# Optimization experiments

Hardware: AMD Instinct MI355X
Metric: run time of the kernel (lower is better)

Reference implementation:

```python
import jax, jax.numpy as jnp
import numpy as np

HEADS = 20          # 1280 / 64 head_dim, standard SD UNet attention
LORA_SCALE = 1.0    # lora_scale init arg


def setup_inputs() -> dict:
    key = jax.random.key(0)
    ks = jax.random.split(key, 16)
    def w(k, shape, s=0.02):
        return jax.random.normal(k, shape, dtype=jnp.float32) * s
    H, C, R = 1280, 768, 64  # hidden_size, cross_attention_dim, lora_rank
    return {
        "hidden_states": jax.random.normal(ks[0], (16, 4096, H), dtype=jnp.float32),
        "encoder_hidden_states": jax.random.normal(ks[1], (16, 77, C), dtype=jnp.float32),
        # base attention projections (diffusers: q/k/v no bias, to_out has bias)
        "Wq": w(ks[2], (H, H)), "Wk": w(ks[3], (C, H)), "Wv": w(ks[4], (C, H)),
        "Wo": w(ks[5], (H, H)), "bo": jnp.zeros((H,), dtype=jnp.float32),
        # LoRA adapters (down: in->rank, up: rank->out, no bias)
        "q_down": w(ks[6], (H, R)), "q_up": w(ks[7], (R, H)),
        "k_down": w(ks[8], (C, R)), "k_up": w(ks[9], (R, H)),
        "v_down": w(ks[10], (C, R)), "v_up": w(ks[11], (R, H)),
        "o_down": w(ks[12], (H, R)), "o_up": w(ks[13], (R, H)),
    }


def reference(hidden_states, encoder_hidden_states, Wq, Wk, Wv, Wo, bo,
              q_down, q_up, k_down, k_up, v_down, v_up, o_down, o_up):
    b, sq, _ = hidden_states.shape
    # base projections + LoRA low-rank corrections
    q = hidden_states @ Wq + LORA_SCALE * ((hidden_states @ q_down) @ q_up)
    k = encoder_hidden_states @ Wk + LORA_SCALE * ((encoder_hidden_states @ k_down) @ k_up)
    v = encoder_hidden_states @ Wv + LORA_SCALE * ((encoder_hidden_states @ v_down) @ v_up)

    d = q.shape[-1] // HEADS
    def split_heads(x):  # [b, s, h*d] -> [b, h, s, d]
        return x.reshape(x.shape[0], x.shape[1], HEADS, d).transpose(0, 2, 1, 3)
    qh, kh, vh = split_heads(q), split_heads(k), split_heads(v)

    # scaled dot-product attention (no mask, non-causal, dropout=0)
    scale = 1.0 / np.sqrt(d).astype(np.float32)
    scores = jnp.einsum('bhqd,bhkd->bhqk', qh, kh) * scale
    probs = jax.nn.softmax(scores, axis=-1)
    attn_out = jnp.einsum('bhqk,bhkd->bhqd', probs, vh)
    attn_out = attn_out.transpose(0, 2, 1, 3).reshape(b, sq, HEADS * d)

    # output projection + LoRA on W_O
    out = attn_out @ Wo + bo + LORA_SCALE * ((attn_out @ o_down) @ o_up)
    return out
```

## Files before the change

kernel.cpp:

```cpp
#include <hip/hip_runtime.h>
#include <stdint.h>

typedef unsigned short u16;
typedef __attribute__((ext_vector_type(8))) short short8;
typedef __attribute__((ext_vector_type(4))) float f32x4;

__device__ __forceinline__ u16 f2bf(float f) {
  union { float f; unsigned u; } v; v.f = f;
  unsigned r = v.u + 0x7fffu + ((v.u >> 16) & 1u);
  return (u16)(r >> 16);
}

__device__ __forceinline__ void g2lds16(const u16* g, u16* l) {
  __builtin_amdgcn_global_load_lds(
      (const __attribute__((address_space(1))) uint32_t*)g,
      (__attribute__((address_space(3))) uint32_t*)l, 16, 0, 0);
}

#define BAR()   asm volatile("s_barrier" ::: "memory")
#define LGKM0() asm volatile("s_waitcnt lgkmcnt(0)" ::: "memory")
#define VM8()   asm volatile("s_waitcnt vmcnt(8)" ::: "memory")
#define VM0()   asm volatile("s_waitcnt vmcnt(0)" ::: "memory")
#define PRIO1() __builtin_amdgcn_s_setprio(1)
#define PRIO0() __builtin_amdgcn_s_setprio(0)

__global__ __launch_bounds__(256) void k_convert(const float* __restrict__ in,
                                                 u16* __restrict__ out, int n8) {
  int i = blockIdx.x * 256 + threadIdx.x;
  if (i >= n8) return;
  const float4* p = (const float4*)(in + (size_t)i * 8);
  float4 a = p[0], b = p[1];
  short8 o;
  o[0] = (short)f2bf(a.x); o[1] = (short)f2bf(a.y);
  o[2] = (short)f2bf(a.z); o[3] = (short)f2bf(a.w);
  o[4] = (short)f2bf(b.x); o[5] = (short)f2bf(b.y);
  o[6] = (short)f2bf(b.z); o[7] = (short)f2bf(b.w);
  *(short8*)(out + (size_t)i * 8) = o;
}

__global__ __launch_bounds__(256) void k_convert_pad(const float* __restrict__ in,
                                                     u16* __restrict__ out,
                                                     int n8_valid, int n8_total) {
  int i = blockIdx.x * 256 + threadIdx.x;
  if (i >= n8_total) return;
  short8 o;
  if (i < n8_valid) {
    const float4* p = (const float4*)(in + (size_t)i * 8);
    float4 a = p[0], b = p[1];
    o[0] = (short)f2bf(a.x); o[1] = (short)f2bf(a.y);
    o[2] = (short)f2bf(a.z); o[3] = (short)f2bf(a.w);
    o[4] = (short)f2bf(b.x); o[5] = (short)f2bf(b.y);
    o[6] = (short)f2bf(b.z); o[7] = (short)f2bf(b.w);
  } else {
#pragma unroll
    for (int e = 0; e < 8; ++e) o[e] = 0;
  }
  *(short8*)(out + (size_t)i * 8) = o;
}

__global__ __launch_bounds__(256) void k_fusew(const float* __restrict__ W,
                                               const float* __restrict__ dn_g,
                                               const float* __restrict__ up_g,
                                               u16* __restrict__ Wt, int K, int N) {
  __shared__ float dn[64][65];
  __shared__ float up[64][17];
  const int k0 = blockIdx.x * 64, n0 = blockIdx.y * 16;
  const int kc = threadIdx.x & 63, ty = threadIdx.x >> 6;
  for (int c = threadIdx.x; c < 4096; c += 256)
    dn[c >> 6][c & 63] = dn_g[(size_t)(k0 + (c >> 6)) * 64 + (c & 63)];
  for (int c = threadIdx.x; c < 1024; c += 256)
    up[c >> 4][c & 15] = up_g[(size_t)(c >> 4) * N + n0 + (c & 15)];
  __syncthreads();
  float acc[4];
#pragma unroll
  for (int e = 0; e < 4; ++e)
    acc[e] = W[(size_t)(k0 + kc) * N + n0 + ty * 4 + e];
#pragma unroll 16
  for (int r = 0; r < 64; ++r) {
    float d = dn[kc][r];
#pragma unroll
    for (int e = 0; e < 4; ++e) acc[e] += d * up[r][ty * 4 + e];
  }
#pragma unroll
  for (int e = 0; e < 4; ++e)
    Wt[(size_t)(n0 + ty * 4 + e) * K + k0 + kc] = f2bf(acc[e]);
}

template <int OUT_MODE>
__global__ __launch_bounds__(256) void k_gemm(const u16* __restrict__ A,
                                              const u16* __restrict__ Bt,
                                              void* __restrict__ Cout,
                                              const float* __restrict__ bias,
                                              int M, int N, int K) {
  __shared__ __align__(16) u16 As[128 * 32];
  __shared__ __align__(16) u16 Bs[128 * 32];
  const int tid = threadIdx.x, lane = tid & 63, w = tid >> 6;
  const int n0 = blockIdx.x * 128, m0 = blockIdx.y * 128;
  const int wm = (w >> 1) * 64, wn = (w & 1) * 64;

  f32x4 acc[4][4];
  f32x4 zf = {0.f, 0.f, 0.f, 0.f};
#pragma unroll
  for (int i = 0; i < 4; ++i)
#pragma unroll
    for (int j = 0; j < 4; ++j) acc[i][j] = zf;

  const int c0 = w, c1 = w + 4;
  const int rA0 = c0 * 16 + (lane >> 2), rA1 = c1 * 16 + (lane >> 2);
  const int kp = (lane & 3) * 8;
  const u16* gA0 = A + (size_t)(m0 + rA0) * K + kp;
  const u16* gA1 = A + (size_t)(m0 + rA1) * K + kp;
  const u16* gB0 = Bt + (size_t)(n0 + rA0) * K + kp;
  const u16* gB1 = Bt + (size_t)(n0 + rA1) * K + kp;
  u16* lA0 = As + c0 * 512;  u16* lA1 = As + c1 * 512;
  u16* lB0 = Bs + c0 * 512;  u16* lB1 = Bs + c1 * 512;

  const int fr = lane & 15, kg = (lane >> 4) * 8;

  for (int k0 = 0; k0 < K; k0 += 32) {
    g2lds16(gA0 + k0, lA0);
    g2lds16(gA1 + k0, lA1);
    g2lds16(gB0 + k0, lB0);
    g2lds16(gB1 + k0, lB1);
    __syncthreads();
    short8 af[4], bf[4];
#pragma unroll
    for (int i = 0; i < 4; ++i)
      af[i] = *(const short8*)(As + (wm + i * 16 + fr) * 32 + kg);
#pragma unroll
    for (int j = 0; j < 4; ++j)
      bf[j] = *(const short8*)(Bs + (wn + j * 16 + fr) * 32 + kg);
#pragma unroll
    for (int i = 0; i < 4; ++i)
#pragma unroll
      for (int j = 0; j < 4; ++j)
        acc[i][j] = __builtin_amdgcn_mfma_f32_16x16x32_bf16(af[i], bf[j], acc[i][j], 0, 0, 0);
    __syncthreads();
  }

  const int rb = (lane >> 4) * 4;
  if (OUT_MODE == 0) {
    u16* C = (u16*)Cout;
#pragma unroll
    for (int i = 0; i < 4; ++i)
#pragma unroll
      for (int j = 0; j < 4; ++j) {
        int col = n0 + wn + j * 16 + fr;
#pragma unroll
        for (int r = 0; r < 4; ++r) {
          int row = m0 + wm + i * 16 + rb + r;
          C[(size_t)row * N + col] = f2bf(acc[i][j][r]);
        }
      }
  } else {
    float* C = (float*)Cout;
#pragma unroll
    for (int i = 0; i < 4; ++i)
#pragma unroll
      for (int j = 0; j < 4; ++j) {
        int col = n0 + wn + j * 16 + fr;
        float bj = bias[col];
#pragma unroll
        for (int r = 0; r < 4; ++r) {
          int row = m0 + wm + i * 16 + rb + r;
          C[(size_t)row * N + col] = acc[i][j][r] + bj;
        }
      }
  }
}


#define GEMM256_SETUP(A_, Bt_)                                                 \
  constexpr int K = 1280;                                                      \
  constexpr int N = 1280;                                                      \
  __shared__ __align__(16) u16 lds[2][2][2][128 * 64];                         \
  const int tid = threadIdx.x, lane = tid & 63, w = tid >> 6;                  \
  const int bid = blockIdx.x;                                                  \
  const int tile = (bid & 7) * 160 + (bid >> 3);                               \
  const int n0 = (tile % 5) * 256, m0 = (tile / 5) * 256;                      \
  const int l0 = w * 2;                                                        \
  const u16* gsrc[8];                                                          \
  _Pragma("unroll") for (int s = 0; s < 8; ++s) {                              \
    const int side = s >> 2, h = (s >> 1) & 1, l = s & 1;                      \
    const int o = (l0 + l) * 1024 + lane * 16;                                 \
    const int row = o >> 7;                                                    \
    const int scol = (o & 127) ^ ((row & 7) << 4);                             \
    const u16* base = side ? ((Bt_) + (size_t)(n0 + h * 128 + row) * K)        \
                           : ((A_) + (size_t)(m0 + h * 128 + row) * K);        \
    gsrc[s] = base + (scol >> 1);                                              \
  }                                                                            \
  const int fr = lane & 15;                                                    \
  const int q16b = (lane >> 4) * 16;                                           \
  const int xr = (fr & 7) << 4;                                                \
  const int cT0 = ((0 + q16b) ^ xr) >> 1;                                      \
  const int cT1 = ((64 + q16b) ^ xr) >> 1;                                     \
  const int ha = w >> 2;                                                       \
  const int hb = (w & 3) >> 1;                                                 \
  const int rB0 = (w & 1) * 64;

#define STAGE(P, KT)                                                           \
  do {                                                                         \
    _Pragma("unroll") for (int s = 0; s < 8; ++s) {                            \
      const int side = s >> 2, h = (s >> 1) & 1, l = s & 1;                    \
      g2lds16(gsrc[s] + (KT) * 64, &lds[P][side][h][(l0 + l) * 512]);          \
    }                                                                          \
  } while (0)

#define LOAD_AF(P, IB)                                                         \
  do {                                                                         \
    _Pragma("unroll") for (int ii = 0; ii < 4; ++ii) {                         \
      const u16* rp = &lds[P][0][ha][(((IB) + ii) * 16 + fr) * 64];            \
      af[ii][0] = *(const short8*)(rp + cT0);                                  \
      af[ii][1] = *(const short8*)(rp + cT1);                                  \
    }                                                                          \
  } while (0)

#define LOAD_BF(P, JB)                                                         \
  do {                                                                         \
    _Pragma("unroll") for (int jj = 0; jj < 2; ++jj) {                         \
      const u16* rp = &lds[P][1][hb][(rB0 + ((JB) + jj) * 16 + fr) * 64];      \
      bf[(JB) + jj][0] = *(const short8*)(rp + cT0);                           \
      bf[(JB) + jj][1] = *(const short8*)(rp + cT1);                           \
    }                                                                          \
  } while (0)

#define MFMA_Q(IO, JB)                                                         \
  do {                                                                         \
    _Pragma("unroll") for (int t = 0; t < 2; ++t)                              \
        _Pragma("unroll") for (int ii = 0; ii < 4; ++ii)                       \
            _Pragma("unroll") for (int jj = 0; jj < 2; ++jj)                   \
                acc[(IO) + ii][(JB) + jj] =                                    \
        __builtin_amdgcn_mfma_f32_16x16x32_bf16(                               \
            af[ii][t], bf[(JB) + jj][t], acc[(IO) + ii][(JB) + jj], 0, 0, 0);  \
  } while (0)

#define GEMM256_EPI()                                                          \
  const int rb = (lane >> 4) * 4;                                              \
  const int orow = m0 + (w >> 2) * 128;                                        \
  const int ocol = n0 + (w & 3) * 64;                                          \
  if (OUT_MODE == 0) {                                                         \
    u16* C = (u16*)Cout;                                                       \
    _Pragma("unroll") for (int i = 0; i < 8; ++i)                              \
        _Pragma("unroll") for (int j = 0; j < 4; ++j) {                        \
      const int col = ocol + j * 16 + fr;                                      \
      _Pragma("unroll") for (int r = 0; r < 4; ++r) {                          \
        const int row = orow + i * 16 + rb + r;                                \
        C[(size_t)row * N + col] = f2bf(acc[i][j][r]);                         \
      }                                                                        \
    }                                                                          \
  } else {                                                                     \
    float* C = (float*)Cout;                                                   \
    _Pragma("unroll") for (int i = 0; i < 8; ++i)                              \
        _Pragma("unroll") for (int j = 0; j < 4; ++j) {                        \
      const int col = ocol + j * 16 + fr;                                      \
      const float bj = bias[col];                                              \
      _Pragma("unroll") for (int r = 0; r < 4; ++r) {                          \
        const int row = orow + i * 16 + rb + r;                                \
        C[(size_t)row * N + col] = acc[i][j][r] + bj;                          \
      }                                                                        \
    }                                                                          \
  }

template <int OUT_MODE>
__global__ __launch_bounds__(512, 2) void k_gemm256(const u16* __restrict__ A,
                                                    const u16* __restrict__ Bt,
                                                    void* __restrict__ Cout,
                                                    const float* __restrict__ bias) {
  GEMM256_SETUP(A, Bt);

  short8 af[4][2], bf[4][2];
  f32x4 acc[8][4];
  {
    f32x4 zf = {0.f, 0.f, 0.f, 0.f};
#pragma unroll
    for (int i = 0; i < 8; ++i)
#pragma unroll
      for (int j = 0; j < 4; ++j) acc[i][j] = zf;
  }

  STAGE(0, 0);
  STAGE(1, 1);
  VM8();
  BAR();

  for (int it = 0; it < 10; ++it) {
    const bool last = (it == 9);
    LOAD_AF(0, 0); LOAD_BF(0, 0);
    BAR(); LGKM0(); PRIO1(); MFMA_Q(0, 0); PRIO0(); BAR();
    LOAD_BF(0, 2);
    BAR(); LGKM0(); PRIO1(); MFMA_Q(0, 2); PRIO0(); BAR();
    LOAD_AF(0, 4);
    BAR(); LGKM0(); PRIO1(); MFMA_Q(4, 2); PRIO0(); BAR();
    if (!last) STAGE(0, 2 * it + 2);
    BAR(); PRIO1(); MFMA_Q(4, 0); PRIO0();
    if (!last) { VM8(); } else { VM0(); }
    BAR();
    LOAD_AF(1, 0); LOAD_BF(1, 0);
    BAR(); LGKM0(); PRIO1(); MFMA_Q(0, 0); PRIO0(); BAR();
    LOAD_BF(1, 2);
    BAR(); LGKM0(); PRIO1(); MFMA_Q(0, 2); PRIO0(); BAR();
    LOAD_AF(1, 4);
    BAR(); LGKM0(); PRIO1(); MFMA_Q(4, 2); PRIO0(); BAR();
    if (!last) STAGE(1, 2 * it + 3);
    BAR(); PRIO1(); MFMA_Q(4, 0); PRIO0();
    if (!last) { VM8(); }
    BAR();
  }

  GEMM256_EPI();
}

template <int OUT_MODE>
__global__ __launch_bounds__(512, 2) void k_gemm256f(const u16* __restrict__ A,
                                                     const u16* __restrict__ Bt,
                                                     void* __restrict__ Cout,
                                                     const float* __restrict__ bias) {
  GEMM256_SETUP(A, Bt);

  short8 af[4][2], bf[4][2];
  f32x4 acc[8][4];
  {
    f32x4 zf = {0.f, 0.f, 0.f, 0.f};
#pragma unroll
    for (int i = 0; i < 8; ++i)
#pragma unroll
      for (int j = 0; j < 4; ++j) acc[i][j] = zf;
  }

  STAGE(0, 0);
  STAGE(1, 1);
  VM8();
  BAR();

  for (int t = 0; t < 20; ++t) {
    const int P = t & 1;
    LOAD_AF(P, 0);
    LOAD_BF(P, 0);
    LOAD_BF(P, 2);
    MFMA_Q(0, 0);
    MFMA_Q(0, 2);
    LOAD_AF(P, 4);
    MFMA_Q(4, 2);
    LGKM0();
    BAR();
    if (t < 18) STAGE(P, t + 2);
    PRIO1(); MFMA_Q(4, 0); PRIO0();
    if (t < 18) { VM8(); } else { VM0(); }
    BAR();
  }

  GEMM256_EPI();
}

__global__ __launch_bounds__(256) void k_attn(u16* __restrict__ Q,
                                              const u16* __restrict__ Kb,
                                              const u16* __restrict__ Vb) {
  const int mt = blockIdx.x, h = blockIdx.y, b = blockIdx.z;
  const int tid = threadIdx.x, lane = tid & 63, w = tid >> 6;
  const int m0 = b * 4096 + mt * 128;
  const int ccol = h * 64;

  __shared__ __align__(16) u16 Kl[80 * 72];
  __shared__ __align__(16) u16 Vt[64 * 104];
  __shared__ __align__(16) u16 Pl[128 * 104];

  {
    short8 z;
#pragma unroll
    for (int e = 0; e < 8; ++e) z[e] = 0;
    for (int i = tid; i < 720; i += 256)  ((short8*)Kl)[i] = z;
    for (int i = tid; i < 832; i += 256)  ((short8*)Vt)[i] = z;
    for (int i = tid; i < 1664; i += 256) ((short8*)Pl)[i] = z;
  }
  __syncthreads();

  for (int c = tid; c < 616; c += 256) {
    int s = c >> 3, d0 = (c & 7) * 8;
    short8 v = *(const short8*)(Kb + (size_t)(b * 77 + s) * 1280 + ccol + d0);
    *(short8*)(Kl + s * 72 + d0) = v;
  }
  for (int c = tid; c < 616; c += 256) {
    int s = c >> 3, d0 = (c & 7) * 8;
    short8 v = *(const short8*)(Vb + (size_t)(b * 77 + s) * 1280 + ccol + d0);
#pragma unroll
    for (int e = 0; e < 8; ++e) Vt[(d0 + e) * 104 + s] = (u16)v[e];
  }

  const int cb = lane & 15, kg = (lane >> 4) * 8;
  short8 qf[2][2];
#pragma unroll
  for (int i = 0; i < 2; ++i)
#pragma unroll
    for (int t = 0; t < 2; ++t) {
      int row = m0 + w * 32 + i * 16 + cb;
      qf[i][t] = *(const short8*)(Q + (size_t)row * 1280 + ccol + t * 32 + kg);
    }
  __syncthreads();

  f32x4 sc[2][5];
  {
    f32x4 zf = {0.f, 0.f, 0.f, 0.f};
#pragma unroll
    for (int i = 0; i < 2; ++i)
#pragma unroll
      for (int j = 0; j < 5; ++j) sc[i][j] = zf;
  }
#pragma unroll
  for (int t = 0; t < 2; ++t) {
    short8 kf[5];
#pragma unroll
    for (int j = 0; j < 5; ++j)
      kf[j] = *(const short8*)(Kl + (j * 16 + cb) * 72 + t * 32 + kg);
#pragma unroll
    for (int i = 0; i < 2; ++i)
#pragma unroll
      for (int j = 0; j < 5; ++j)
        sc[i][j] = __builtin_amdgcn_mfma_f32_16x16x32_bf16(qf[i][t], kf[j], sc[i][j], 0, 0, 0);
  }

  float inv[2][4];
#pragma unroll
  for (int i = 0; i < 2; ++i) {
#pragma unroll
    for (int r = 0; r < 4; ++r) {
      float m = -1e30f;
#pragma unroll
      for (int j = 0; j < 5; ++j) {
        float s = sc[i][j][r] * 0.125f;
        sc[i][j][r] = s;
        if (j * 16 + cb < 77) m = fmaxf(m, s);
      }
#pragma unroll
      for (int mk = 8; mk >= 1; mk >>= 1) m = fmaxf(m, __shfl_xor(m, mk, 64));
      float sum = 0.f;
#pragma unroll
      for (int j = 0; j < 5; ++j) {
        float pv = (j * 16 + cb < 77) ? __expf(sc[i][j][r] - m) : 0.f;
        sc[i][j][r] = pv;
        sum += pv;
      }
#pragma unroll
      for (int mk = 8; mk >= 1; mk >>= 1) sum += __shfl_xor(sum, mk, 64);
      inv[i][r] = 1.f / sum;
    }
  }

  {
    int rbase = (lane >> 4) * 4;
#pragma unroll
    for (int i = 0; i < 2; ++i)
#pragma unroll
      for (int j = 0; j < 5; ++j)
#pragma unroll
        for (int r = 0; r < 4; ++r)
          Pl[(w * 32 + i * 16 + rbase + r) * 104 + j * 16 + cb] = f2bf(sc[i][j][r]);
  }
  __syncthreads();

  f32x4 o[2][4];
  {
    f32x4 zf = {0.f, 0.f, 0.f, 0.f};
#pragma unroll
    for (int i = 0; i < 2; ++i)
#pragma unroll
      for (int n = 0; n < 4; ++n) o[i][n] = zf;
  }
#pragma unroll
  for (int t = 0; t < 3; ++t) {
    short8 pf[2], vf[4];
#pragma unroll
    for (int i = 0; i < 2; ++i)
      pf[i] = *(const short8*)(Pl + (w * 32 + i * 16 + cb) * 104 + t * 32 + kg);
#pragma unroll
    for (int n = 0; n < 4; ++n)
      vf[n] = *(const short8*)(Vt + (n * 16 + cb) * 104 + t * 32 + kg);
#pragma unroll
    for (int i = 0; i < 2; ++i)
#pragma unroll
      for (int n = 0; n < 4; ++n)
        o[i][n] = __builtin_amdgcn_mfma_f32_16x16x32_bf16(pf[i], vf[n], o[i][n], 0, 0, 0);
  }

  {
    int rbase = (lane >> 4) * 4;
#pragma unroll
    for (int i = 0; i < 2; ++i)
#pragma unroll
      for (int n = 0; n < 4; ++n)
#pragma unroll
        for (int r = 0; r < 4; ++r) {
          int row = m0 + w * 32 + i * 16 + rbase + r;
          Q[(size_t)row * 1280 + ccol + n * 16 + cb] = f2bf(o[i][n][r] * inv[i][r]);
        }
  }
}

extern "C" void kernel_launch(void* const* d_in, const int* in_sizes, int n_in,
                              void* d_out, int out_size, void* d_ws, size_t ws_size,
                              hipStream_t stream) {
  (void)in_sizes; (void)n_in; (void)out_size; (void)ws_size;
  const float* hs  = (const float*)d_in[0];
  const float* ehs = (const float*)d_in[1];
  const float* Wq  = (const float*)d_in[2];
  const float* Wk  = (const float*)d_in[3];
  const float* Wv  = (const float*)d_in[4];
  const float* Wo  = (const float*)d_in[5];
  const float* bo  = (const float*)d_in[6];
  const float* qd  = (const float*)d_in[7];
  const float* qu  = (const float*)d_in[8];
  const float* kd  = (const float*)d_in[9];
  const float* ku  = (const float*)d_in[10];
  const float* vd  = (const float*)d_in[11];
  const float* vu  = (const float*)d_in[12];
  const float* od  = (const float*)d_in[13];
  const float* ou  = (const float*)d_in[14];

  char* p = (char*)d_ws;
  u16* q_buf = (u16*)p;  p += (size_t)65536 * 1280 * 2;
  u16* wq_t  = (u16*)p;  p += (size_t)1280 * 1280 * 2;
  u16* wo_t  = (u16*)p;  p += (size_t)1280 * 1280 * 2;
  u16* wk_t  = (u16*)p;  p += (size_t)1280 * 768 * 2;
  u16* wv_t  = (u16*)p;  p += (size_t)1280 * 768 * 2;
  u16* ehs_b = (u16*)p;  p += (size_t)1280 * 768 * 2;
  u16* k_buf = (u16*)p;  p += (size_t)1280 * 1280 * 2;
  u16* v_buf = (u16*)p;  p += (size_t)1280 * 1280 * 2;
  u16* hs_b  = (u16*)d_out;

  k_convert<<<40960, 256, 0, stream>>>(hs, hs_b, 10485760);
  k_convert_pad<<<480, 256, 0, stream>>>(ehs, ehs_b, 118272, 122880);

  k_fusew<<<dim3(20, 80), 256, 0, stream>>>(Wq, qd, qu, wq_t, 1280, 1280);
  k_fusew<<<dim3(12, 80), 256, 0, stream>>>(Wk, kd, ku, wk_t, 768, 1280);
  k_fusew<<<dim3(12, 80), 256, 0, stream>>>(Wv, vd, vu, wv_t, 768, 1280);
  k_fusew<<<dim3(20, 80), 256, 0, stream>>>(Wo, od, ou, wo_t, 1280, 1280);

  k_gemm256f<0><<<1280, 512, 0, stream>>>(hs_b, wq_t, q_buf, nullptr);
  k_gemm<0><<<dim3(10, 10), 256, 0, stream>>>(ehs_b, wk_t, k_buf, nullptr, 1280, 1280, 768);
  k_gemm<0><<<dim3(10, 10), 256, 0, stream>>>(ehs_b, wv_t, v_buf, nullptr, 1280, 1280, 768);

  k_attn<<<dim3(32, 20, 16), 256, 0, stream>>>(q_buf, k_buf, v_buf);

  k_gemm256<1><<<1280, 512, 0, stream>>>(q_buf, wo_t, d_out, bo);
}
```

Baseline: 803.2 us.

## Fuse fp32-to-bf16 conversion into Q GEMM and fold softmax scale into Q

Removes the standalone hidden_states conversion kernel by having the Q projection GEMM load fp32 A tiles, convert them to bf16 in registers, and write them to LDS. The softmax scale and log2(e) factor are applied in the Q GEMM epilogue, so the attention kernel can use exp2f without the row-max reduction. This cuts a full pass over the large input. Risks are a slower A-load path than direct global-to-LDS loads, and possible overflow because the max subtraction is gone.

```diff
diff --git a/kernel.cpp b/kernel.cpp
--- a/kernel.cpp
+++ b/kernel.cpp
@@ -1,4 +1,5 @@
 #include <hip/hip_runtime.h>
+#include <hip/hip_bf16.h>
 #include <stdint.h>
 
 typedef unsigned short u16;
@@ -9,6 +10,13 @@
   union { float f; unsigned u; } v; v.f = f;
   unsigned r = v.u + 0x7fffu + ((v.u >> 16) & 1u);
   return (u16)(r >> 16);
+}
+
+__device__ __forceinline__ unsigned pkbf2(float lo, float hi) {
+  __hip_bfloat162 h2 = __float22bfloat162_rn(make_float2(lo, hi));
+  unsigned u;
+  __builtin_memcpy(&u, &h2, sizeof(u));
+  return u;
 }
 
 __device__ __forceinline__ void g2lds16(const u16* g, u16* l) {
@@ -24,19 +32,7 @@
 #define PRIO1() __builtin_amdgcn_s_setprio(1)
 #define PRIO0() __builtin_amdgcn_s_setprio(0)
 
-__global__ __launch_bounds__(256) void k_convert(const float* __restrict__ in,
-                                                 u16* __restrict__ out, int n8) {
-  int i = blockIdx.x * 256 + threadIdx.x;
-  if (i >= n8) return;
-  const float4* p = (const float4*)(in + (size_t)i * 8);
-  float4 a = p[0], b = p[1];
-  short8 o;
-  o[0] = (short)f2bf(a.x); o[1] = (short)f2bf(a.y);
-  o[2] = (short)f2bf(a.z); o[3] = (short)f2bf(a.w);
-  o[4] = (short)f2bf(b.x); o[5] = (short)f2bf(b.y);
-  o[6] = (short)f2bf(b.z); o[7] = (short)f2bf(b.w);
-  *(short8*)(out + (size_t)i * 8) = o;
-}
+#define QSCALE 0.18033688f
 
 __global__ __launch_bounds__(256) void k_convert_pad(const float* __restrict__ in,
                                                      u16* __restrict__ out,
@@ -170,25 +166,15 @@
 }
 
 
-#define GEMM256_SETUP(A_, Bt_)                                                 \
+#define GEMM256_TILE_RD()                                                      \
   constexpr int K = 1280;                                                      \
   constexpr int N = 1280;                                                      \
   __shared__ __align__(16) u16 lds[2][2][2][128 * 64];                         \
-  const int tid = threadIdx.x, lane = tid & 63, w = tid >> 6;                  \
+  const int lane = threadIdx.x & 63, w = threadIdx.x >> 6;                     \
   const int bid = blockIdx.x;                                                  \
   const int tile = (bid & 7) * 160 + (bid >> 3);                               \
   const int n0 = (tile % 5) * 256, m0 = (tile / 5) * 256;                      \
   const int l0 = w * 2;                                                        \
-  const u16* gsrc[8];                                                          \
-  _Pragma("unroll") for (int s = 0; s < 8; ++s) {                              \
-    const int side = s >> 2, h = (s >> 1) & 1, l = s & 1;                      \
-    const int o = (l0 + l) * 1024 + lane * 16;                                 \
-    const int row = o >> 7;                                                    \
-    const int scol = (o & 127) ^ ((row & 7) << 4);                             \
-    const u16* base = side ? ((Bt_) + (size_t)(n0 + h * 128 + row) * K)        \
-                           : ((A_) + (size_t)(m0 + h * 128 + row) * K);        \
-    gsrc[s] = base + (scol >> 1);                                              \
-  }                                                                            \
   const int fr = lane & 15;                                                    \
   const int q16b = (lane >> 4) * 16;                                           \
   const int xr = (fr & 7) << 4;                                                \
@@ -198,14 +184,6 @@
   const int hb = (w & 3) >> 1;                                                 \
   const int rB0 = (w & 1) * 64;
 
-#define STAGE(P, KT)                                                           \
-  do {                                                                         \
-    _Pragma("unroll") for (int s = 0; s < 8; ++s) {                            \
-      const int side = s >> 2, h = (s >> 1) & 1, l = s & 1;                    \
-      g2lds16(gsrc[s] + (KT) * 64, &lds[P][side][h][(l0 + l) * 512]);          \
-    }                                                                          \
-  } while (0)
-
 #define LOAD_AF(P, IB)                                                         \
   do {                                                                         \
     _Pragma("unroll") for (int ii = 0; ii < 4; ++ii) {                         \
@@ -234,98 +212,42 @@
             af[ii][t], bf[(JB) + jj][t], acc[(IO) + ii][(JB) + jj], 0, 0, 0);  \
   } while (0)
 
-#define GEMM256_EPI()                                                          \
-  const int rb = (lane >> 4) * 4;                                              \
-  const int orow = m0 + (w >> 2) * 128;                                        \
-  const int ocol = n0 + (w & 3) * 64;                                          \
-  if (OUT_MODE == 0) {                                                         \
-    u16* C = (u16*)Cout;                                                       \
+#define ACC_ZERO()                                                             \
+  do {                                                                         \
+    f32x4 zf = {0.f, 0.f, 0.f, 0.f};                                           \
     _Pragma("unroll") for (int i = 0; i < 8; ++i)                              \
-        _Pragma("unroll") for (int j = 0; j < 4; ++j) {                        \
-      const int col = ocol + j * 16 + fr;                                      \
-      _Pragma("unroll") for (int r = 0; r < 4; ++r) {                          \
-        const int row = orow + i * 16 + rb + r;                                \
-        C[(size_t)row * N + col] = f2bf(acc[i][j][r]);                         \
-      }                                                                        \
-    }                                                                          \
-  } else {                                                                     \
-    float* C = (float*)Cout;                                                   \
-    _Pragma("unroll") for (int i = 0; i < 8; ++i)                              \
-        _Pragma("unroll") for (int j = 0; j < 4; ++j) {                        \
-      const int col = ocol + j * 16 + fr;                                      \
-      const float bj = bias[col];                                              \
-      _Pragma("unroll") for (int r = 0; r < 4; ++r) {                          \
-        const int row = orow + i * 16 + rb + r;                                \
-        C[(size_t)row * N + col] = acc[i][j][r] + bj;                          \
-      }                                                                        \
-    }                                                                          \
-  }
-
-template <int OUT_MODE>
-__global__ __launch_bounds__(512, 2) void k_gemm256(const u16* __restrict__ A,
-                                                    const u16* __restrict__ Bt,
-                                                    void* __restrict__ Cout,
-                                                    const float* __restrict__ bias) {
-  GEMM256_SETUP(A, Bt);
-
-  short8 af[4][2], bf[4][2];
-  f32x4 acc[8][4];
-  {
-    f32x4 zf = {0.f, 0.f, 0.f, 0.f};
-#pragma unroll
-    for (int i = 0; i < 8; ++i)
-#pragma unroll
-      for (int j = 0; j < 4; ++j) acc[i][j] = zf;
-  }
-
-  STAGE(0, 0);
-  STAGE(1, 1);
-  VM8();
-  BAR();
-
-  for (int it = 0; it < 10; ++it) {
-    const bool last = (it == 9);
-    LOAD_AF(0, 0); LOAD_BF(0, 0);
-    BAR(); LGKM0(); PRIO1(); MFMA_Q(0, 0); PRIO0(); BAR();
-    LOAD_BF(0, 2);
-    BAR(); LGKM0(); PRIO1(); MFMA_Q(0, 2); PRIO0(); BAR();
-    LOAD_AF(0, 4);
-    BAR(); LGKM0(); PRIO1(); MFMA_Q(4, 2); PRIO0(); BAR();
-    if (!last) STAGE(0, 2 * it + 2);
-    BAR(); PRIO1(); MFMA_Q(4, 0); PRIO0();
-    if (!last) { VM8(); } else { VM0(); }
-    BAR();
-    LOAD_AF(1, 0); LOAD_BF(1, 0);
-    BAR(); LGKM0(); PRIO1(); MFMA_Q(0, 0); PRIO0(); BAR();
-    LOAD_BF(1, 2);
-    BAR(); LGKM0(); PRIO1(); MFMA_Q(0, 2); PRIO0(); BAR();
-    LOAD_AF(1, 4);
-    BAR(); LGKM0(); PRIO1(); MFMA_Q(4, 2); PRIO0(); BAR();
-    if (!last) STAGE(1, 2 * it + 3);
-    BAR(); PRIO1(); MFMA_Q(4, 0); PRIO0();
-    if (!last) { VM8(); }
-    BAR();
-  }
-
-  GEMM256_EPI();
-}
+        _Pragma("unroll") for (int j = 0; j < 4; ++j) acc[i][j] = zf;          \
+  } while (0)
 
 template <int OUT_MODE>
 __global__ __launch_bounds__(512, 2) void k_gemm256f(const u16* __restrict__ A,
                                                      const u16* __restrict__ Bt,
                                                      void* __restrict__ Cout,
                                                      const float* __restrict__ bias) {
-  GEMM256_SETUP(A, Bt);
+  GEMM256_TILE_RD();
+  const u16* gsrc[8];
+#pragma unroll
+  for (int s = 0; s < 8; ++s) {
+    const int side = s >> 2, h = (s >> 1) & 1, l = s & 1;
+    const int o = (l0 + l) * 1024 + lane * 16;
+    const int row = o >> 7;
+    const int scol = (o & 127) ^ ((row & 7) << 4);
+    const u16* base = side ? (Bt + (size_t)(n0 + h * 128 + row) * K)
+                           : (A + (size_t)(m0 + h * 128 + row) * K);
+    gsrc[s] = base + (scol >> 1);
+  }
+
+#define STAGE(P, KT)                                                           \
+  do {                                                                         \
+    _Pragma("unroll") for (int s = 0; s < 8; ++s) {                            \
+      const int side = s >> 2, h = (s >> 1) & 1, l = s & 1;                    \
+      g2lds16(gsrc[s] + (KT) * 64, &lds[P][side][h][(l0 + l) * 512]);          \
+    }                                                                          \
+  } while (0)
 
   short8 af[4][2], bf[4][2];
   f32x4 acc[8][4];
-  {
-    f32x4 zf = {0.f, 0.f, 0.f, 0.f};
-#pragma unroll
-    for (int i = 0; i < 8; ++i)
-#pragma unroll
-      for (int j = 0; j < 4; ++j) acc[i][j] = zf;
-  }
+  ACC_ZERO();
 
   STAGE(0, 0);
   STAGE(1, 1);
@@ -348,8 +270,139 @@
     if (t < 18) { VM8(); } else { VM0(); }
     BAR();
   }
-
-  GEMM256_EPI();
+#undef STAGE
+
+  const int rb = (lane >> 4) * 4;
+  const int orow = m0 + (w >> 2) * 128;
+  const int ocol = n0 + (w & 3) * 64;
+  if (OUT_MODE == 0) {
+    u16* C = (u16*)Cout;
+#pragma unroll
+    for (int i = 0; i < 8; ++i)
+#pragma unroll
+      for (int j = 0; j < 4; ++j) {
+        const int col = ocol + j * 16 + fr;
+#pragma unroll
+        for (int r = 0; r < 4; ++r)
+          C[(size_t)(orow + i * 16 + rb + r) * N + col] = f2bf(acc[i][j][r]);
+      }
+  } else {
+    float* C = (float*)Cout;
+#pragma unroll
+    for (int i = 0; i < 8; ++i)
+#pragma unroll
+      for (int j = 0; j < 4; ++j) {
+        const int col = ocol + j * 16 + fr;
+        const float bj = bias[col];
+#pragma unroll
+        for (int r = 0; r < 4; ++r)
+          C[(size_t)(orow + i * 16 + rb + r) * N + col] = acc[i][j][r] + bj;
+      }
+  }
+}
+
+__global__ __launch_bounds__(512, 2) void k_gemm256q(const float* __restrict__ A,
+                                                     const u16* __restrict__ Bt,
+                                                     u16* __restrict__ Cout) {
+  GEMM256_TILE_RD();
+  const u16* gB[4];
+#pragma unroll
+  for (int s = 0; s < 4; ++s) {
+    const int h = s >> 1, l = s & 1;
+    const int o = (l0 + l) * 1024 + lane * 16;
+    const int row = o >> 7;
+    const int scol = (o & 127) ^ ((row & 7) << 4);
+    gB[s] = Bt + (size_t)(n0 + h * 128 + row) * K + (scol >> 1);
+  }
+  const float* gA[4];
+  int aoff[4];
+#pragma unroll
+  for (int s = 0; s < 4; ++s) {
+    const int h = s >> 1, l = s & 1;
+    const int o = (l0 + l) * 1024 + lane * 16;
+    const int row = o >> 7;
+    gA[s] = A + (size_t)(m0 + h * 128 + row) * K + ((o & 127) >> 1);
+    aoff[s] = row * 64 + (((o & 127) ^ ((row & 7) << 4)) >> 1);
+  }
+
+#define ALOADQ(KT)                                                             \
+  do {                                                                         \
+    _Pragma("unroll") for (int s = 0; s < 4; ++s) {                            \
+      const float4* p_ = (const float4*)(gA[s] + (KT) * 64);                   \
+      av[s][0] = p_[0];                                                        \
+      av[s][1] = p_[1];                                                        \
+    }                                                                          \
+  } while (0)
+
+#define ASTOREQ(P)                                                             \
+  do {                                                                         \
+    _Pragma("unroll") for (int s = 0; s < 4; ++s) {                            \
+      uint4 pk_;                                                               \
+      pk_.x = pkbf2(av[s][0].x, av[s][0].y);                                   \
+      pk_.y = pkbf2(av[s][0].z, av[s][0].w);                                   \
+      pk_.z = pkbf2(av[s][1].x, av[s][1].y);                                   \
+      pk_.w = pkbf2(av[s][1].z, av[s][1].w);                                   \
+      *(uint4*)(&lds[(P)][0][s >> 1][aoff[s]]) = pk_;                          \
+    }                                                                          \
+  } while (0)
+
+#define BSTAGEQ(P, KT)                                                         \
+  do {                                                                         \
+    _Pragma("unroll") for (int s = 0; s < 4; ++s)                              \
+      g2lds16(gB[s] + (KT) * 64, &lds[(P)][1][s >> 1][(l0 + (s & 1)) * 512]);  \
+  } while (0)
+
+  short8 af[4][2], bf[4][2];
+  f32x4 acc[8][4];
+  float4 av[4][2];
+  ACC_ZERO();
+
+  ALOADQ(0); ASTOREQ(0); BSTAGEQ(0, 0);
+  ALOADQ(1); ASTOREQ(1); BSTAGEQ(1, 1);
+  ALOADQ(2);
+  VM0();
+  LGKM0();
+  BAR();
+
+  for (int t = 0; t < 20; ++t) {
+    const int P = t & 1;
+    LOAD_AF(P, 0);
+    LOAD_BF(P, 0);
+    LOAD_BF(P, 2);
+    MFMA_Q(0, 0);
+    MFMA_Q(0, 2);
+    LOAD_AF(P, 4);
+    MFMA_Q(4, 2);
+    LGKM0();
+    BAR();
+    if (t < 18) {
+      VM0();
+      ASTOREQ(P);
+      BSTAGEQ(P, t + 2);
+      if (t < 17) ALOADQ(t + 3);
+    } else if (t == 18) {
+      VM0();
+    }
+    PRIO1(); MFMA_Q(4, 0); PRIO0();
+    LGKM0();
+    BAR();
+  }
+#undef ALOADQ
+#undef ASTOREQ
+#undef BSTAGEQ
+
+  const int rb = (lane >> 4) * 4;
+  const int orow = m0 + (w >> 2) * 128;
+  const int ocol = n0 + (w & 3) * 64;
+#pragma unroll
+  for (int i = 0; i < 8; ++i)
+#pragma unroll
+    for (int j = 0; j < 4; ++j) {
+      const int col = ocol + j * 16 + fr;
+#pragma unroll
+      for (int r = 0; r < 4; ++r)
+        Cout[(size_t)(orow + i * 16 + rb + r) * N + col] = f2bf(acc[i][j][r] * QSCALE);
+    }
 }
 
 __global__ __launch_bounds__(256) void k_attn(u16* __restrict__ Q,
@@ -423,20 +476,16 @@
   for (int i = 0; i < 2; ++i) {
 #pragma unroll
     for (int r = 0; r < 4; ++r) {
-      float m = -1e30f;
-#pragma unroll
-      for (int j = 0; j < 5; ++j) {
-        float s = sc[i][j][r] * 0.125f;
-        sc[i][j][r] = s;
-        if (j * 16 + cb < 77) m = fmaxf(m, s);
+      float sum = 0.f;
+#pragma unroll
+      for (int j = 0; j < 4; ++j) {
+        float pv = exp2f(sc[i][j][r]);
+        sc[i][j][r] = pv;
+        sum += pv;
       }
-#pragma unroll
-      for (int mk = 8; mk >= 1; mk >>= 1) m = fmaxf(m, __shfl_xor(m, mk, 64));
-      float sum = 0.f;
-#pragma unroll
-      for (int j = 0; j < 5; ++j) {
-        float pv = (j * 16 + cb < 77) ? __expf(sc[i][j][r] - m) : 0.f;
-        sc[i][j][r] = pv;
+      {
+        float pv = (cb < 13) ? exp2f(sc[i][4][r]) : 0.f;
+        sc[i][4][r] = pv;
         sum += pv;
       }
 #pragma unroll
@@ -524,9 +573,7 @@
   u16* ehs_b = (u16*)p;  p += (size_t)1280 * 768 * 2;
   u16* k_buf = (u16*)p;  p += (size_t)1280 * 1280 * 2;
   u16* v_buf = (u16*)p;  p += (size_t)1280 * 1280 * 2;
-  u16* hs_b  = (u16*)d_out;
-
-  k_convert<<<40960, 256, 0, stream>>>(hs, hs_b, 10485760);
+
   k_convert_pad<<<480, 256, 0, stream>>>(ehs, ehs_b, 118272, 122880);
 
   k_fusew<<<dim3(20, 80), 256, 0, stream>>>(Wq, qd, qu, wq_t, 1280, 1280);
@@ -534,11 +581,11 @@
   k_fusew<<<dim3(12, 80), 256, 0, stream>>>(Wv, vd, vu, wv_t, 768, 1280);
   k_fusew<<<dim3(20, 80), 256, 0, stream>>>(Wo, od, ou, wo_t, 1280, 1280);
 
-  k_gemm256f<0><<<1280, 512, 0, stream>>>(hs_b, wq_t, q_buf, nullptr);
+  k_gemm256q<<<1280, 512, 0, stream>>>(hs, wq_t, q_buf);
   k_gemm<0><<<dim3(10, 10), 256, 0, stream>>>(ehs_b, wk_t, k_buf, nullptr, 1280, 1280, 768);
   k_gemm<0><<<dim3(10, 10), 256, 0, stream>>>(ehs_b, wv_t, v_buf, nullptr, 1280, 1280, 768);
 
   k_attn<<<dim3(32, 20, 16), 256, 0, stream>>>(q_buf, k_buf, v_buf);
 
-  k_gemm256<1><<<1280, 512, 0, stream>>>(q_buf, wo_t, d_out, bo);
-}
+  k_gemm256f<1><<<1280, 512, 0, stream>>>(q_buf, wo_t, d_out, bo);
+}
```

Result: faster. 755.3 us (-6.0%).
